# Optimization experiments

Measured on AMD Instinct MI355X. Metric: run time of the kernel, lower is better.

The kernel has to match this reference:

```python
import jax, jax.numpy as jnp
import numpy as np

N_NODES = 50000
N_EDGES = 800000
DIM = 128
N_LAYERS = 2          # num_layers - 1 GIN layers
NUM_GRAPHS = 512      # rows of the sparse graph_pool matrix
BN_EPS = 1e-5


def setup_inputs() -> dict:
    key = jax.random.key(0)
    ks = jax.random.split(key, 10)
    x = jax.random.normal(ks[0], (N_NODES, DIM), dtype=jnp.float32)
    edge_src = jax.random.randint(ks[1], (N_EDGES,), 0, N_NODES, dtype=jnp.int32)
    edge_dst = jax.random.randint(ks[2], (N_EDGES,), 0, N_NODES, dtype=jnp.int32)
    edge_weight = jax.random.uniform(ks[3], (N_EDGES,), dtype=jnp.float32)
    graph_ids = jnp.sort(jax.random.randint(ks[4], (N_NODES,), 0, NUM_GRAPHS, dtype=jnp.int32))
    pool_w = jnp.ones((N_NODES,), dtype=jnp.float32)
    scale = 1.0 / np.sqrt(DIM)
    W1 = jax.random.normal(ks[5], (N_LAYERS, DIM, DIM), dtype=jnp.float32) * scale
    b1 = jnp.zeros((N_LAYERS, DIM), dtype=jnp.float32)
    W2 = jax.random.normal(ks[6], (N_LAYERS, DIM, DIM), dtype=jnp.float32) * scale
    b2 = jnp.zeros((N_LAYERS, DIM), dtype=jnp.float32)
    bn_gamma = jnp.ones((N_LAYERS, DIM), dtype=jnp.float32)
    bn_beta = jnp.zeros((N_LAYERS, DIM), dtype=jnp.float32)
    return {"x": x, "edge_src": edge_src, "edge_dst": edge_dst,
            "edge_weight": edge_weight, "graph_ids": graph_ids, "pool_w": pool_w,
            "W1": W1, "b1": b1, "W2": W2, "b2": b2,
            "bn_gamma": bn_gamma, "bn_beta": bn_beta}


def reference(x, edge_src, edge_dst, edge_weight, graph_ids, pool_w,
              W1, b1, W2, b2, bn_gamma, bn_beta):
    h = x
    n = h.shape[0]
    for l in range(N_LAYERS):
        # pooled = adj @ h, adj in COO form: adj[dst, src] = edge_weight
        msg = edge_weight[:, None] * h[edge_src]                    # [E, D] gather
        pooled = jax.ops.segment_sum(msg, edge_dst, num_segments=n) # [N, D] scatter-add
        # 2-linear MLP (num_mlp_layers=2): Linear -> ReLU -> Linear
        hid = jax.nn.relu(pooled @ W1[l] + b1[l])
        z = hid @ W2[l] + b2[l]
        # BatchNorm1d over the node dimension (training-mode batch stats)
        mu = jnp.mean(z, axis=0)
        var = jnp.mean(jnp.square(z - mu), axis=0)
        z = bn_gamma[l] * (z - mu) * jax.lax.rsqrt(var + BN_EPS) + bn_beta[l]
        h = jax.nn.relu(z)
    x_nodes = h
    # pooled_x = graph_pool @ h, graph_pool[g, i] = pool_w[i] for node i in graph g
    pooled_x = jax.ops.segment_sum(pool_w[:, None] * h, graph_ids,
                                   num_segments=NUM_GRAPHS)
    return pooled_x, x_nodes
```

## Files before the change

kernel.cpp:

```cpp
#include <hip/hip_runtime.h>

#define N_NODES    50000
#define N_EDGES    800000
#define DIM        128
#define NUM_GRAPHS 512
#define BN_EPS     1e-5f

#define NBUCK      196
#define TILE       4096
#define MLP_ROWS   128
#define POOL_SPLIT 4

typedef unsigned int u32;
typedef unsigned short u16;
typedef __attribute__((ext_vector_type(8))) short bf16x8;
typedef __attribute__((ext_vector_type(4))) float f32x4;

__device__ __forceinline__ u16 f2bf(float f) {
    u32 u = __float_as_uint(f);
    u += 0x7FFF + ((u >> 16) & 1);
    return (u16)(u >> 16);
}
__device__ __forceinline__ float bf2f(u16 h) {
    return __uint_as_float((u32)h << 16);
}

__global__ __launch_bounds__(256)
void fill_zero2_kernel(float* __restrict__ p1, int n1, float* __restrict__ p2, int n2)
{
    int stride = gridDim.x * blockDim.x;
    for (int i = blockIdx.x * 256 + threadIdx.x; i < n1 + n2; i += stride) {
        if (i < n1) p1[i] = 0.f;
        else        p2[i - n1] = 0.f;
    }
}

__global__ __launch_bounds__(256)
void prep_kernel(const float* __restrict__ x, const float* __restrict__ W1,
                 const float* __restrict__ W2, const int* __restrict__ dst,
                 u16* __restrict__ hx, u16* __restrict__ wt,
                 int* __restrict__ bucketCnt)
{
    if (blockIdx.x < 256) {
        int idx = blockIdx.x * 256 + threadIdx.x;
        int m    = idx >> 14;
        int f    = idx & 16383;
        int c    = (f >> 11) & 7;
        int kk   = (f >> 9) & 3;
        int lane = (f >> 3) & 63;
        int e    = f & 7;
        int k = kk * 32 + ((lane >> 4) << 3) + e;
        int j = c * 16 + (lane & 15);
        const float* src = (m & 1) ? W2 : W1;
        src += (m >> 1) * 128 * 128;
        wt[idx] = f2bf(src[k * 128 + j]);
    } else if (blockIdx.x < 1280) {
        const long long n4 = (long long)N_NODES * DIM / 4;
        long long stride = 1024LL * 256;
        for (long long i = (blockIdx.x - 256) * 256LL + threadIdx.x; i < n4; i += stride) {
            float4 v = ((const float4*)x)[i];
            ushort4 o;
            o.x = f2bf(v.x); o.y = f2bf(v.y); o.z = f2bf(v.z); o.w = f2bf(v.w);
            ((ushort4*)hx)[i] = o;
        }
    } else {
        __shared__ int cnt[NBUCK];
        int t = threadIdx.x;
        if (t < NBUCK) cnt[t] = 0;
        __syncthreads();
        int stride = 256 * 256;
        for (int i = (blockIdx.x - 1280) * 256 + t; i < N_EDGES / 4; i += stride) {
            int4 d = ((const int4*)dst)[i];
            atomicAdd(&cnt[d.x >> 8], 1);
            atomicAdd(&cnt[d.y >> 8], 1);
            atomicAdd(&cnt[d.z >> 8], 1);
            atomicAdd(&cnt[d.w >> 8], 1);
        }
        __syncthreads();
        if (t < NBUCK && cnt[t] > 0) atomicAdd(&bucketCnt[t], cnt[t]);
    }
}

__global__ __launch_bounds__(512)
void partitionA(const int* __restrict__ src, const int* __restrict__ dst,
                const float* __restrict__ ew, const int* __restrict__ bucketCnt,
                int* __restrict__ gCursor, uint2* __restrict__ ed2)
{
    __shared__ int bstart[NBUCK];
    __shared__ int cnt[NBUCK];
    __shared__ int off[NBUCK];
    __shared__ int gb[NBUCK];
    __shared__ u32 stg_sw[TILE];
    __shared__ u32 stg_d[TILE];
    __shared__ int scanb[256];

    const int t = threadIdx.x;
    const int base = blockIdx.x * TILE;
    const int tcnt = min(TILE, N_EDGES - base);

    {
        int v = (t < NBUCK) ? bucketCnt[t] : 0;
        if (t < 256) scanb[t] = v;
        __syncthreads();
        for (int o = 1; o < 256; o <<= 1) {
            int x = (t < 256 && t >= o) ? scanb[t - o] : 0;
            __syncthreads();
            if (t < 256) scanb[t] += x;
            __syncthreads();
        }
        if (t < NBUCK) { bstart[t] = scanb[t] - v; cnt[t] = 0; }
    }
    __syncthreads();

    u32 swv[8], dv[8];
    int rk[8], bk[8];
    #pragma unroll
    for (int j = 0; j < 8; ++j) {
        int e = base + j * 512 + t;
        if (e < N_EDGES) {
            int d = dst[e];
            swv[j] = ((u32)f2bf(ew[e]) << 16) | (u32)src[e];
            dv[j]  = (u32)d;
            bk[j]  = d >> 8;
            rk[j]  = atomicAdd(&cnt[bk[j]], 1);
        } else bk[j] = -1;
    }
    __syncthreads();

    {
        int v = (t < NBUCK) ? cnt[t] : 0;
        if (t < 256) scanb[t] = v;
        __syncthreads();
        for (int o = 1; o < 256; o <<= 1) {
            int x = (t < 256 && t >= o) ? scanb[t - o] : 0;
            __syncthreads();
            if (t < 256) scanb[t] += x;
            __syncthreads();
        }
        if (t < NBUCK) off[t] = scanb[t] - v;
    }
    __syncthreads();

    #pragma unroll
    for (int j = 0; j < 8; ++j) {
        if (bk[j] >= 0) {
            int idx = off[bk[j]] + rk[j];
            stg_sw[idx] = swv[j];
            stg_d[idx]  = dv[j];
        }
    }
    if (t < NBUCK && cnt[t] > 0) gb[t] = atomicAdd(&gCursor[t], cnt[t]);
    __syncthreads();

    for (int j = t; j < tcnt; j += 512) {
        u32 d = stg_d[j];
        int b = (int)(d >> 8);
        int pos = bstart[b] + gb[b] + (j - off[b]);
        ed2[pos] = make_uint2(stg_sw[j], d);
    }
}

__global__ __launch_bounds__(256)
void partitionB(const uint2* __restrict__ ed2, const int* __restrict__ bucketCnt,
                int* __restrict__ rowptr, u32* __restrict__ ed)
{
    __shared__ int bstart[256];
    __shared__ int hist[256];
    __shared__ int sc[256];
    __shared__ int cur[256];

    const int b = blockIdx.x;
    const int t = threadIdx.x;

    {
        int v = (t < NBUCK) ? bucketCnt[t] : 0;
        sc[t] = v;
        __syncthreads();
        for (int o = 1; o < 256; o <<= 1) {
            int x = (t >= o) ? sc[t - o] : 0;
            __syncthreads();
            sc[t] += x;
            __syncthreads();
        }
        bstart[t] = sc[t] - v;
    }
    __syncthreads();

    const int s = bstart[b];
    const int n = bucketCnt[b];

    hist[t] = 0;
    __syncthreads();
    for (int j = t; j < n; j += 256)
        atomicAdd(&hist[ed2[s + j].y & 255u], 1);
    __syncthreads();

    int v = hist[t];
    sc[t] = v;
    __syncthreads();
    for (int o = 1; o < 256; o <<= 1) {
        int x = (t >= o) ? sc[t - o] : 0;
        __syncthreads();
        sc[t] += x;
        __syncthreads();
    }
    int excl = sc[t] - v;
    rowptr[b * 256 + t] = s + excl;
    cur[t] = s + excl;
    __syncthreads();

    for (int j = t; j < n; j += 256) {
        uint2 r = ed2[s + j];
        int d = (int)(r.y & 255u);
        int p = atomicAdd(&cur[d], 1);
        ed[p] = r.x;
    }
}

template<bool BN>
__global__ __launch_bounds__(256)
void gather_spmm(const u16* __restrict__ h, const u32* __restrict__ ed,
                 const int* __restrict__ rowptr, u16* __restrict__ pooled,
                 const float* __restrict__ stats, const float* __restrict__ gamma,
                 const float* __restrict__ beta)
{
    __shared__ float scs[128];
    __shared__ float shs[128];
    if (BN) {
        if (threadIdx.x < 128) {
            int c = threadIdx.x;
            float mu  = stats[c] * (1.f / N_NODES);
            float var = stats[128 + c] * (1.f / N_NODES) - mu * mu;
            float s   = gamma[c] * rsqrtf(var + BN_EPS);
            scs[c] = s;
            shs[c] = beta[c] - mu * s;
        }
        __syncthreads();
    }

    int node = blockIdx.x * 16 + (threadIdx.x >> 4);
    int lane = threadIdx.x & 15;
    int beg = rowptr[node];
    int end = rowptr[node + 1];

    float sc8[8], sh8[8];
    if (BN) {
        #pragma unroll
        for (int q = 0; q < 8; ++q) {
            sc8[q] = scs[lane * 8 + q];
            sh8[q] = shs[lane * 8 + q];
        }
    }

    float acc[8];
    #pragma unroll
    for (int q = 0; q < 8; ++q) acc[q] = 0.f;

    u32 sw_cur = (beg + lane < end) ? ed[beg + lane] : 0u;
    for (int base = beg; base < end; base += 16) {
        u32 sw_next = (base + 16 + lane < end) ? ed[base + 16 + lane] : 0u;
        int cnt = min(16, end - base);
        #pragma unroll 4
        for (int i = 0; i < cnt; ++i) {
            u32 rec = __shfl(sw_cur, i, 16);
            long long s = (long long)(rec & 0xFFFFu);
            float w = bf2f((u16)(rec >> 16));
            bf16x8 hv = *((const bf16x8*)(h + (s << 7)) + lane);
            #pragma unroll
            for (int q = 0; q < 8; ++q) {
                float v = bf2f((u16)hv[q]);
                if (BN) v = fmaxf(v * sc8[q] + sh8[q], 0.f);
                acc[q] += w * v;
            }
        }
        sw_cur = sw_next;
    }
    bf16x8 o;
    #pragma unroll
    for (int q = 0; q < 8; ++q) o[q] = (short)f2bf(acc[q]);
    *((bf16x8*)(pooled + ((long long)node << 7)) + lane) = o;
}

__global__ __launch_bounds__(512)
void fused_mlp(const u16* __restrict__ A, const u16* __restrict__ wtL,
               const float* __restrict__ b1, const float* __restrict__ b2,
               u16* __restrict__ Z, float* __restrict__ stats)
{
    __shared__ __align__(16) u16 wfrag[32768];
    __shared__ float ssum[128];
    __shared__ float ssq[128];

    const int tid  = threadIdx.x;
    const int lane = tid & 63;
    const int wave = tid >> 6;
    const int l15  = lane & 15;
    const int lk   = lane >> 4;
    const int row0 = blockIdx.x * MLP_ROWS;
    const int wrow = wave * 16;

    #pragma unroll
    for (int i = 0; i < 8; ++i) {
        int idx = tid + i * 512;
        *(bf16x8*)&wfrag[idx * 8] = *(const bf16x8*)(wtL + idx * 8);
    }
    if (tid < 128) { ssum[tid] = 0.f; ssq[tid] = 0.f; }

    bf16x8 afr[4];
    {
        int rg = row0 + wrow + l15;
        bool ok = rg < N_NODES;
        const u16* ap = A + (long long)rg * 128 + lk * 8;
        bf16x8 zero = {};
        #pragma unroll
        for (int kk = 0; kk < 4; ++kk)
            afr[kk] = ok ? *(const bf16x8*)(ap + kk * 32) : zero;
    }
    __syncthreads();

    f32x4 acc1[8];
    #pragma unroll
    for (int c = 0; c < 8; ++c) {
        float bv = b1[c * 16 + l15];
        f32x4 a = {bv, bv, bv, bv};
        #pragma unroll
        for (int kk = 0; kk < 4; ++kk) {
            bf16x8 w = *(bf16x8*)&wfrag[((c * 4 + kk) * 64 + lane) * 8];
            a = __builtin_amdgcn_mfma_f32_16x16x32_bf16(afr[kk], w, a, 0, 0, 0);
        }
        acc1[c] = a;
    }
    __syncthreads();

    #pragma unroll
    for (int c = 0; c < 8; ++c) {
        #pragma unroll
        for (int i = 0; i < 4; ++i) {
            int row = wrow + lk * 4 + i;
            int col = c * 16 + l15;
            wfrag[row * 128 + (col ^ ((row & 15) << 3))] = f2bf(fmaxf(acc1[c][i], 0.f));
        }
    }

    bf16x8 afr2[4];
    {
        int row = wrow + l15;
        #pragma unroll
        for (int kk = 0; kk < 4; ++kk)
            afr2[kk] = *(bf16x8*)&wfrag[row * 128 + ((kk * 32 + lk * 8) ^ ((row & 15) << 3))];
    }

    #pragma unroll
    for (int c = 0; c < 8; ++c) {
        float bv = b2[c * 16 + l15];
        f32x4 a = {bv, bv, bv, bv};
        #pragma unroll
        for (int kk = 0; kk < 4; ++kk) {
            bf16x8 w = *(bf16x8*)&wfrag[16384 + ((c * 4 + kk) * 64 + lane) * 8];
            a = __builtin_amdgcn_mfma_f32_16x16x32_bf16(afr2[kk], w, a, 0, 0, 0);
        }
        float s = 0.f, sq = 0.f;
        #pragma unroll
        for (int i = 0; i < 4; ++i) {
            int row = wrow + lk * 4 + i;
            int rg  = row0 + row;
            float v = a[i];
            bool ok = rg < N_NODES;
            if (ok) { s += v; sq += v * v; }
            wfrag[row * 128 + ((c * 16 + l15) ^ ((row & 15) << 3))] = ok ? f2bf(v) : (u16)0;
        }
        s  += __shfl_xor(s, 16);  s  += __shfl_xor(s, 32);
        sq += __shfl_xor(sq, 16); sq += __shfl_xor(sq, 32);
        if (lk == 0) {
            atomicAdd(&ssum[c * 16 + l15], s);
            atomicAdd(&ssq[c * 16 + l15], sq);
        }
    }

    #pragma unroll
    for (int j = 0; j < 4; ++j) {
        int chunk = j * 64 + lane;
        int rl  = chunk >> 4;
        int c8  = chunk & 15;
        int row = wrow + rl;
        int rg  = row0 + row;
        if (rg < N_NODES) {
            bf16x8 v = *(bf16x8*)&wfrag[row * 128 + ((c8 * 8) ^ ((row & 15) << 3))];
            *(bf16x8*)(Z + (long long)rg * 128 + c8 * 8) = v;
        }
    }
    __syncthreads();
    if (tid < 128) {
        atomicAdd(&stats[tid], ssum[tid]);
        atomicAdd(&stats[128 + tid], ssq[tid]);
    }
}

__global__ __launch_bounds__(256)
void graph_pool_bn(const u16* __restrict__ z, const float* __restrict__ stats,
                   const float* __restrict__ gamma, const float* __restrict__ beta,
                   const int* __restrict__ gid, const float* __restrict__ pw,
                   float* __restrict__ out_nodes, float* __restrict__ out_pool)
{
    __shared__ float scs[128];
    __shared__ float shs[128];
    if (threadIdx.x < 128) {
        int c = threadIdx.x;
        float mu  = stats[c] * (1.f / N_NODES);
        float var = stats[128 + c] * (1.f / N_NODES) - mu * mu;
        float s   = gamma[c] * rsqrtf(var + BN_EPS);
        scs[c] = s;
        shs[c] = beta[c] - mu * s;
    }
    __syncthreads();

    int g    = blockIdx.x >> 2;
    int part = blockIdx.x & 3;

    int lo = 0, hi = N_NODES;
    while (lo < hi) { int m = (lo + hi) >> 1; if (gid[m] < g) lo = m + 1; else hi = m; }
    int start = lo;
    hi = N_NODES;
    while (lo < hi) { int m = (lo + hi) >> 1; if (gid[m] < g + 1) lo = m + 1; else hi = m; }
    int end = lo;

    int len  = end - start;
    int qlen = (len + 3) >> 2;
    int s = start + part * qlen;
    int e = min(end, s + qlen);

    const int t  = threadIdx.x;
    const int rg = t >> 5;
    const int c4 = t & 31;
    float4 sc4 = *(float4*)&scs[c4 * 4];
    float4 sh4 = *(float4*)&shs[c4 * 4];

    float4 acc = make_float4(0.f, 0.f, 0.f, 0.f);
    for (int r = s + rg; r < e; r += 8) {
        float w = pw[r];
        ushort4 hv = *((const ushort4*)(z + (long long)r * DIM) + c4);
        float4 v;
        v.x = fmaxf(bf2f(hv.x) * sc4.x + sh4.x, 0.f);
        v.y = fmaxf(bf2f(hv.y) * sc4.y + sh4.y, 0.f);
        v.z = fmaxf(bf2f(hv.z) * sc4.z + sh4.z, 0.f);
        v.w = fmaxf(bf2f(hv.w) * sc4.w + sh4.w, 0.f);
        *((float4*)(out_nodes + (long long)r * DIM) + c4) = v;
        acc.x += w * v.x; acc.y += w * v.y;
        acc.z += w * v.z; acc.w += w * v.w;
    }

    __shared__ float4 sd[256];
    sd[t] = acc;
    __syncthreads();
    if (t < 32) {
        float4 tot = sd[t];
        #pragma unroll
        for (int i = 1; i < 8; ++i) {
            float4 v = sd[i * 32 + t];
            tot.x += v.x; tot.y += v.y; tot.z += v.z; tot.w += v.w;
        }
        float* op = out_pool + g * DIM + t * 4;
        atomicAdd(op + 0, tot.x);
        atomicAdd(op + 1, tot.y);
        atomicAdd(op + 2, tot.z);
        atomicAdd(op + 3, tot.w);
    }
}

extern "C" void kernel_launch(void* const* d_in, const int* in_sizes, int n_in,
                              void* d_out, int out_size, void* d_ws, size_t ws_size,
                              hipStream_t stream)
{
    const float* x    = (const float*)d_in[0];
    const int*   esrc = (const int*)d_in[1];
    const int*   edst = (const int*)d_in[2];
    const float* ew   = (const float*)d_in[3];
    const int*   gid  = (const int*)d_in[4];
    const float* pw   = (const float*)d_in[5];
    const float* W1   = (const float*)d_in[6];
    const float* b1   = (const float*)d_in[7];
    const float* W2   = (const float*)d_in[8];
    const float* b2   = (const float*)d_in[9];
    const float* gam  = (const float*)d_in[10];
    const float* bet  = (const float*)d_in[11];

    float* out_pool  = (float*)d_out;
    float* out_nodes = (float*)d_out + NUM_GRAPHS * DIM;

    const size_t NF = (size_t)N_NODES * DIM;
    char* w = (char*)d_ws;
    uint2* ed2      = (uint2*)w;      w += (size_t)N_EDGES * sizeof(uint2);
    u32*   ed       = (u32*)w;        w += (size_t)N_EDGES * sizeof(u32);
    u16*   pooledBf = (u16*)w;        w += NF * sizeof(u16);
    u16*   zBf      = (u16*)w;        w += NF * sizeof(u16);
    u16*   hx       = (u16*)w;        w += NF * sizeof(u16);
    u16*   wt       = (u16*)w;        w += (size_t)4 * 128 * 128 * sizeof(u16);
    float* stats0   = (float*)w;      w += 256 * sizeof(float);
    float* stats1   = (float*)w;      w += 256 * sizeof(float);
    int*   bucketCnt= (int*)w;        w += 256 * sizeof(int);
    int*   gCursor  = (int*)w;        w += 256 * sizeof(int);
    int*   rowptr   = (int*)w;        w += (NBUCK * 256 + 64) * sizeof(int);

    const int mlpGrid    = (N_NODES + MLP_ROWS - 1) / MLP_ROWS;
    const int gatherGrid = (N_NODES + 15) / 16;
    const int partGrid   = (N_EDGES + TILE - 1) / TILE;

    fill_zero2_kernel<<<64, 256, 0, stream>>>(stats0, 1024,
                                              out_pool, NUM_GRAPHS * DIM);
    prep_kernel<<<1536, 256, 0, stream>>>(x, W1, W2, edst, hx, wt, bucketCnt);
    partitionA<<<partGrid, 512, 0, stream>>>(esrc, edst, ew, bucketCnt, gCursor, ed2);
    partitionB<<<NBUCK, 256, 0, stream>>>(ed2, bucketCnt, rowptr, ed);

    gather_spmm<false><<<gatherGrid, 256, 0, stream>>>(hx, ed, rowptr, pooledBf,
                                                       nullptr, nullptr, nullptr);
    fused_mlp<<<mlpGrid, 512, 0, stream>>>(pooledBf, wt, b1, b2, zBf, stats0);

    gather_spmm<true><<<gatherGrid, 256, 0, stream>>>(zBf, ed, rowptr, pooledBf,
                                                      stats0, gam, bet);
    fused_mlp<<<mlpGrid, 512, 0, stream>>>(pooledBf, wt + 32768,
                                           b1 + DIM, b2 + DIM, zBf, stats1);

    graph_pool_bn<<<NUM_GRAPHS * POOL_SPLIT, 256, 0, stream>>>(
        zBf, stats1, gam + DIM, bet + DIM, gid, pw, out_nodes, out_pool);
}
```

Measured before the change: 166.4 us.

## Drop bucket-count pass using fixed-capacity buckets and sub-sort edges by source

```diff
diff --git a/kernel.cpp b/kernel.cpp
--- a/kernel.cpp
+++ b/kernel.cpp
@@ -7,6 +7,8 @@
 #define BN_EPS     1e-5f
 
 #define NBUCK      196
+#define CAP        4608
+#define NBINS      2048
 #define TILE       4096
 #define MLP_ROWS   128
 #define POOL_SPLIT 4
@@ -37,9 +39,8 @@
 
 __global__ __launch_bounds__(256)
 void prep_kernel(const float* __restrict__ x, const float* __restrict__ W1,
-                 const float* __restrict__ W2, const int* __restrict__ dst,
-                 u16* __restrict__ hx, u16* __restrict__ wt,
-                 int* __restrict__ bucketCnt)
+                 const float* __restrict__ W2, u16* __restrict__ hx,
+                 u16* __restrict__ wt)
 {
     if (blockIdx.x < 256) {
         int idx = blockIdx.x * 256 + threadIdx.x;
@@ -54,7 +55,7 @@
         const float* src = (m & 1) ? W2 : W1;
         src += (m >> 1) * 128 * 128;
         wt[idx] = f2bf(src[k * 128 + j]);
-    } else if (blockIdx.x < 1280) {
+    } else {
         const long long n4 = (long long)N_NODES * DIM / 4;
         long long stride = 1024LL * 256;
         for (long long i = (blockIdx.x - 256) * 256LL + threadIdx.x; i < n4; i += stride) {
@@ -63,30 +64,14 @@
             o.x = f2bf(v.x); o.y = f2bf(v.y); o.z = f2bf(v.z); o.w = f2bf(v.w);
             ((ushort4*)hx)[i] = o;
         }
-    } else {
-        __shared__ int cnt[NBUCK];
-        int t = threadIdx.x;
-        if (t < NBUCK) cnt[t] = 0;
-        __syncthreads();
-        int stride = 256 * 256;
-        for (int i = (blockIdx.x - 1280) * 256 + t; i < N_EDGES / 4; i += stride) {
-            int4 d = ((const int4*)dst)[i];
-            atomicAdd(&cnt[d.x >> 8], 1);
-            atomicAdd(&cnt[d.y >> 8], 1);
-            atomicAdd(&cnt[d.z >> 8], 1);
-            atomicAdd(&cnt[d.w >> 8], 1);
-        }
-        __syncthreads();
-        if (t < NBUCK && cnt[t] > 0) atomicAdd(&bucketCnt[t], cnt[t]);
     }
 }
 
 __global__ __launch_bounds__(512)
 void partitionA(const int* __restrict__ src, const int* __restrict__ dst,
-                const float* __restrict__ ew, const int* __restrict__ bucketCnt,
-                int* __restrict__ gCursor, uint2* __restrict__ ed2)
-{
-    __shared__ int bstart[NBUCK];
+                const float* __restrict__ ew, int* __restrict__ gCursor,
+                uint2* __restrict__ ed2)
+{
     __shared__ int cnt[NBUCK];
     __shared__ int off[NBUCK];
     __shared__ int gb[NBUCK];
@@ -98,18 +83,7 @@
     const int base = blockIdx.x * TILE;
     const int tcnt = min(TILE, N_EDGES - base);
 
-    {
-        int v = (t < NBUCK) ? bucketCnt[t] : 0;
-        if (t < 256) scanb[t] = v;
-        __syncthreads();
-        for (int o = 1; o < 256; o <<= 1) {
-            int x = (t < 256 && t >= o) ? scanb[t - o] : 0;
-            __syncthreads();
-            if (t < 256) scanb[t] += x;
-            __syncthreads();
-        }
-        if (t < NBUCK) { bstart[t] = scanb[t] - v; cnt[t] = 0; }
-    }
+    if (t < NBUCK) cnt[t] = 0;
     __syncthreads();
 
     u32 swv[8], dv[8];
@@ -155,25 +129,25 @@
     for (int j = t; j < tcnt; j += 512) {
         u32 d = stg_d[j];
         int b = (int)(d >> 8);
-        int pos = bstart[b] + gb[b] + (j - off[b]);
+        long long pos = (long long)b * CAP + gb[b] + (j - off[b]);
         ed2[pos] = make_uint2(stg_sw[j], d);
     }
 }
 
 __global__ __launch_bounds__(256)
-void partitionB(const uint2* __restrict__ ed2, const int* __restrict__ bucketCnt,
+void partitionB(const uint2* __restrict__ ed2, const int* __restrict__ gCursor,
                 int* __restrict__ rowptr, u32* __restrict__ ed)
 {
     __shared__ int bstart[256];
-    __shared__ int hist[256];
+    __shared__ int hist[NBINS];
+    __shared__ int cursor[NBINS];
     __shared__ int sc[256];
-    __shared__ int cur[256];
 
     const int b = blockIdx.x;
     const int t = threadIdx.x;
 
     {
-        int v = (t < NBUCK) ? bucketCnt[t] : 0;
+        int v = (t < NBUCK) ? gCursor[t] : 0;
         sc[t] = v;
         __syncthreads();
         for (int o = 1; o < 256; o <<= 1) {
@@ -186,17 +160,24 @@
     }
     __syncthreads();
 
-    const int s = bstart[b];
-    const int n = bucketCnt[b];
-
-    hist[t] = 0;
-    __syncthreads();
-    for (int j = t; j < n; j += 256)
-        atomicAdd(&hist[ed2[s + j].y & 255u], 1);
-    __syncthreads();
-
-    int v = hist[t];
-    sc[t] = v;
+    const int s0 = bstart[b];
+    const int n  = gCursor[b];
+    const uint2* srcp = ed2 + (long long)b * CAP;
+
+    #pragma unroll
+    for (int q = 0; q < 8; ++q) hist[t + q * 256] = 0;
+    __syncthreads();
+    for (int j = t; j < n; j += 256) {
+        uint2 r = srcp[j];
+        int bin = (int)((r.y & 255u) << 3) | (int)((r.x & 0xFFFFu) >> 13);
+        atomicAdd(&hist[bin], 1);
+    }
+    __syncthreads();
+
+    int loc[8]; int sum = 0;
+    #pragma unroll
+    for (int q = 0; q < 8; ++q) { loc[q] = hist[t * 8 + q]; sum += loc[q]; }
+    sc[t] = sum;
     __syncthreads();
     for (int o = 1; o < 256; o <<= 1) {
         int x = (t >= o) ? sc[t - o] : 0;
@@ -204,15 +185,19 @@
         sc[t] += x;
         __syncthreads();
     }
-    int excl = sc[t] - v;
-    rowptr[b * 256 + t] = s + excl;
-    cur[t] = s + excl;
+    int run = sc[t] - sum;
+    rowptr[b * 256 + t] = s0 + run;
+    #pragma unroll
+    for (int q = 0; q < 8; ++q) {
+        cursor[t * 8 + q] = s0 + run;
+        run += loc[q];
+    }
     __syncthreads();
 
     for (int j = t; j < n; j += 256) {
-        uint2 r = ed2[s + j];
-        int d = (int)(r.y & 255u);
-        int p = atomicAdd(&cur[d], 1);
+        uint2 r = srcp[j];
+        int bin = (int)((r.y & 255u) << 3) | (int)((r.x & 0xFFFFu) >> 13);
+        int p = atomicAdd(&cursor[bin], 1);
         ed[p] = r.x;
     }
 }
@@ -488,7 +473,6 @@
 
     const size_t NF = (size_t)N_NODES * DIM;
     char* w = (char*)d_ws;
-    uint2* ed2      = (uint2*)w;      w += (size_t)N_EDGES * sizeof(uint2);
     u32*   ed       = (u32*)w;        w += (size_t)N_EDGES * sizeof(u32);
     u16*   pooledBf = (u16*)w;        w += NF * sizeof(u16);
     u16*   zBf      = (u16*)w;        w += NF * sizeof(u16);
@@ -496,19 +480,20 @@
     u16*   wt       = (u16*)w;        w += (size_t)4 * 128 * 128 * sizeof(u16);
     float* stats0   = (float*)w;      w += 256 * sizeof(float);
     float* stats1   = (float*)w;      w += 256 * sizeof(float);
-    int*   bucketCnt= (int*)w;        w += 256 * sizeof(int);
     int*   gCursor  = (int*)w;        w += 256 * sizeof(int);
     int*   rowptr   = (int*)w;        w += (NBUCK * 256 + 64) * sizeof(int);
+
+    uint2* ed2cap   = (uint2*)pooledBf;
 
     const int mlpGrid    = (N_NODES + MLP_ROWS - 1) / MLP_ROWS;
     const int gatherGrid = (N_NODES + 15) / 16;
     const int partGrid   = (N_EDGES + TILE - 1) / TILE;
 
-    fill_zero2_kernel<<<64, 256, 0, stream>>>(stats0, 1024,
+    fill_zero2_kernel<<<64, 256, 0, stream>>>(stats0, 768,
                                               out_pool, NUM_GRAPHS * DIM);
-    prep_kernel<<<1536, 256, 0, stream>>>(x, W1, W2, edst, hx, wt, bucketCnt);
-    partitionA<<<partGrid, 512, 0, stream>>>(esrc, edst, ew, bucketCnt, gCursor, ed2);
-    partitionB<<<NBUCK, 256, 0, stream>>>(ed2, bucketCnt, rowptr, ed);
+    prep_kernel<<<1280, 256, 0, stream>>>(x, W1, W2, hx, wt);
+    partitionA<<<partGrid, 512, 0, stream>>>(esrc, edst, ew, gCursor, ed2cap);
+    partitionB<<<NBUCK, 256, 0, stream>>>(ed2cap, gCursor, rowptr, ed);
 
     gather_spmm<false><<<gatherGrid, 256, 0, stream>>>(hx, ed, rowptr, pooledBf,
                                                        nullptr, nullptr, nullptr);
```

Result: faster. 157.5 us, median of 2 (-5.4%).
